# Optimization experiments

Measured on AMD Instinct MI355X. Metric: run time of the kernel, lower is better.

Reference implementation:

```python
import jax, jax.numpy as jnp
import numpy as np

# ParamsJR('JR') defaults, all variances 0 -> fixed constants; w_bb and lm are the fit params.
DT = 1e-4                      # step_size
VMAX, V0, R = 5.0, 6.0, 0.56   # sigmoid params
U_UB = 500.0                   # u_2ndsys_ub
G_EFF = 0.01 + 1000.0          # lb + relu(g)
C1_EFF, C2_EFF = 0.01 + 135.0, 0.01 + 135.0 * 0.8
C3_EFF, C4_EFF = 0.01 + 135.0 * 0.25, 0.01 + 135.0 * 0.25
STD_EFF = 150.0 + 100.0        # noise_std_lb + relu(std_in)
K_EFF = 0.5 + 5.0              # k_lb + relu(k)
A_EFF, a_EFF = 3.25, 1.0 + 100.0   # 0+relu(A), 1+relu(a)
B_EFF, b_EFF = 22.0, 1.0 + 50.0    # 0+relu(B), 1+relu(b)
CY0, Y0, MU = 5.0, 2.0, 0.5
CONDUCT_LB = 1.5


def _sig(x):
    return VMAX / (1.0 + jnp.exp(R * (V0 - x)))


def _sys2nd(A, a, u, x, v):
    return A * a * u - 2.0 * a * v - a * a * x


def _sat(x):  # state saturation 1000*tanh(x/1000)
    return 1000.0 * jnp.tanh(x / 1000.0)


def setup_inputs() -> dict:
    N, H, B, OUT, BUF = 200, 20, 400, 64, 500
    key = jax.random.key(0)
    ks = jax.random.split(key, 7)
    return {
        "input": jax.random.normal(ks[0], (N, H, B), jnp.float32),
        "noise_in": jax.random.normal(ks[1], (N, H, B, 3), jnp.float32),
        "noise_out": jax.random.normal(ks[2], (N, B), jnp.float32),
        "hx": jax.random.uniform(ks[3], (N, 6), jnp.float32),
        "hE": jnp.zeros((N, BUF), jnp.float32),
        "w_bb": jnp.full((N, N), 0.05, jnp.float32),  # zeros + 0.05 init
        "lm": jax.random.normal(ks[4], (OUT, N), jnp.float32),
        "sc": jax.random.uniform(ks[5], (N, N), jnp.float32),
        "dist": jax.random.randint(ks[6], (N, N), 0, 100, dtype=jnp.int32),
    }


def _forward(input, noise_in, noise_out, hx, hE, w_bb, lm, sc, delays):
    OUT = lm.shape[0]
    # connectivity normalization (done once, outside the time loop, as in torch)
    w = jnp.exp(w_bb) * sc
    wl = jnp.log1p(0.5 * (w + w.T))
    w_n = wl / jnp.linalg.norm(wl)             # (N,N)
    dg = -jnp.diag(jnp.sum(w_n, axis=1))       # (N,N) Laplacian diagonal
    # lead-field normalization: rowwise L1 (torch: sqrt(lm**2).sum(1)), then column mean-center
    lm1 = lm / jnp.abs(lm).sum(axis=1, keepdims=True)
    lm_t = lm1 - lm1.sum(axis=0, keepdims=True) / OUT

    def inner(carry, xs):
        M, E, I, Mv, Ev, Iv, hEb = carry
        u, nE = xs                                              # (N,1) each
        Ed = jnp.take_along_axis(hEb, delays, axis=1)           # delayed M buffer
        LEd = jnp.sum(w_n * Ed.T, axis=1, keepdims=True)        # (N,1)
        rM = _sig(E - I)
        rE = STD_EFF * nE + G_EFF * (LEd + dg @ E) + C2_EFF * _sig(C1_EFF * M)
        rI = C4_EFF * _sig(C3_EFF * M)
        ddM = M + DT * Mv
        ddE = E + DT * Ev
        ddI = I + DT * Iv
        ddMv = Mv + DT * _sys2nd(A_EFF, a_EFF, U_UB * jnp.tanh(rM / U_UB), M, Mv)
        ddEv = Ev + DT * _sys2nd(A_EFF, a_EFF, K_EFF * u + U_UB * jnp.tanh(rE / U_UB), E, Ev)
        ddIv = Iv + DT * _sys2nd(B_EFF, b_EFF, U_UB * jnp.tanh(rI / U_UB), I, Iv)
        M, E, I = _sat(ddM), _sat(ddE), _sat(ddI)
        Mv, Ev, Iv = _sat(ddMv), _sat(ddEv), _sat(ddIv)
        hEb = hEb.at[:, 0].set(M[:, 0])
        return (M, E, I, Mv, Ev, Iv, hEb), None

    def outer(carry, xs):
        u_tr, n_tr = xs                                         # (H,N,1) each
        carry, _ = jax.lax.scan(inner, carry, (u_tr, n_tr))
        M, E, I, Mv, Ev, Iv, hEb = carry
        hEb = jnp.concatenate([M, hEb[:, :-1]], axis=1)         # shift delay buffer per TR
        eeg = CY0 * (lm_t @ (E - I)) - Y0                       # (OUT,1)
        return (M, E, I, Mv, Ev, Iv, hEb), eeg[:, 0]

    M, E, I = hx[:, 0:1], hx[:, 1:2], hx[:, 2:3]
    Mv, Ev, Iv = hx[:, 3:4], hx[:, 4:5], hx[:, 5:6]
    u_all = jnp.transpose(input, (2, 1, 0))[..., None]          # (B,H,N,1)
    nE_all = jnp.transpose(noise_in[..., 0], (2, 1, 0))[..., None]
    carry, eeg = jax.lax.scan(outer, (M, E, I, Mv, Ev, Iv, hE), (u_all, nE_all))
    M, E, I, Mv, Ev, Iv, _ = carry
    current_state = jnp.concatenate([M, E, I, Mv, Ev, Iv], axis=1)  # (N,6)
    return eeg.T, current_state                                 # eeg_batch (OUT,B)


def reference(input, noise_in, noise_out, hx, hE, w_bb, lm, sc, dist):
    delays = (dist.astype(jnp.float32) / (CONDUCT_LB + MU)).astype(jnp.int32)
    return _forward(input, noise_in, noise_out, hx, hE, w_bb, lm, sc, delays)
```

## Files before the change

kernel.cpp:

```cpp
#include <hip/hip_runtime.h>
#include <math.h>

namespace {

constexpr int N_   = 200;
constexpr int H_   = 20;
constexpr int B_   = 400;
constexpr int OUT_ = 64;
constexpr int BUF_ = 500;
constexpr int NT_  = 1024;
constexpr int HD_  = 50;
constexpr int HS_  = 51;
constexpr int GT0  = 224;
constexpr int NG_  = 800;
constexpr int EPT  = 50;
constexpr int CAP  = 16;
constexpr int UNR  = 12;

constexpr float L2E = 1.4426950408889634f;
constexpr float LN2 = 0.6931471805599453f;

constexpr float DT_  = 0.0001f;
constexpr float G_   = 1000.01f;
constexpr float C1_  = 135.01f;
constexpr float C2_  = 108.01f;
constexpr float C3_  = 33.76f;
constexpr float C4_  = 33.76f;
constexpr float STD_ = 250.0f;
constexpr float K_   = 5.5f;
constexpr float CY0_ = 5.0f;
constexpr float Y0_  = 2.0f;

constexpr float RL2E = 0.56f * L2E;
constexpr float V0R  = 6.0f * RL2E;
constexpr float TU_  = 2.0f * L2E / 500.0f;
constexpr float TS_  = 2.0f * L2E / 1000.0f;

constexpr float KMv = 0.9798f, KMu = 0.0328250f, KMx = 1.0201f;
constexpr float KEv = 0.9798f, KEu = 0.0328250f, KEx = 1.0201f;
constexpr float KIv = 0.9898f, KIu = 0.1122000f, KIx = 0.2601f;

__device__ __forceinline__ float fexp2(float x){ return __builtin_amdgcn_exp2f(x); }
__device__ __forceinline__ float flog2(float x){ return __builtin_amdgcn_logf(x); }
__device__ __forceinline__ float frcp (float x){ return __builtin_amdgcn_rcpf(x); }

__device__ __forceinline__ float sigf(float x){
    return 5.0f * frcp(1.0f + fexp2(fmaf(-RL2E, x, V0R)));
}
__device__ __forceinline__ float tanh500(float x){
    return 500.0f - 1000.0f * frcp(1.0f + fexp2(x * TU_));
}
__device__ __forceinline__ float satf(float x){
    return 1000.0f - 2000.0f * frcp(1.0f + fexp2(x * TS_));
}
__device__ __forceinline__ float wl_f(const float* __restrict__ wbb,
                                      const float* __restrict__ sc,
                                      int i, int j){
    float w0 = fexp2(wbb[i*N_+j]*L2E) * sc[i*N_+j];
    float w1 = fexp2(wbb[j*N_+i]*L2E) * sc[j*N_+i];
    return flog2(1.0f + 0.5f*(w0+w1)) * LN2;
}

__global__ void __launch_bounds__(NT_)
jansen_kernel(
    const float* __restrict__ input,
    const float* __restrict__ noise_in,
    const float* __restrict__ hx,
    const float* __restrict__ hEin,
    const float* __restrict__ wbb,
    const float* __restrict__ lm,
    const float* __restrict__ sc,
    const int*   __restrict__ dist,
    float* __restrict__ out,
    float2* __restrict__ tab)
{
    __shared__ float histT[N_*HS_];
    __shared__ float uslab[H_*N_];
    __shared__ float neslab[H_*N_];
    __shared__ float d0w_l[CAP*N_];
    __shared__ unsigned char d0j_l[CAP*N_];
    __shared__ float d1w_l[CAP*N_];
    __shared__ unsigned char d1j_l[CAP*N_];
    __shared__ float led_part[4*N_];
    __shared__ float mcol[2*N_];
    __shared__ float emi[N_];
    __shared__ float colmean[N_];
    __shared__ float lmrs[OUT_];
    __shared__ float red_s[NT_/64];
    __shared__ float norm_s;

    const int t = threadIdx.x;
    const bool isr = (t < N_);
    const bool isg = (t >= GT0);
    const int  gt  = t - GT0;
    const int  grow  = gt >> 2;
    const int  gslot = gt & 3;
    const int  jbase = gslot * EPT;
    const int  tb    = gt * EPT;

    int sidx[5];
    int goff[5];

    if (t < OUT_){
        float s2 = 0.f;
        for (int j=0;j<N_;++j) s2 += fabsf(lm[t*N_+j]);
        lmrs[t] = s2;
    }
    float M=0,E=0,I=0,Mv=0,Ev=0,Iv=0, rowsum=0, ledst=0;
    int cnt0=0, cnt1=0;
    #pragma unroll
    for (int r=0;r<5;++r){ sidx[r]=0; goff[r]=0; }
    if (isg){
        #pragma unroll
        for (int r=0;r<5;++r){
            int p = r*NG_ + gt;
            int hh = p / N_, ii = p - hh*N_;
            sidx[r] = hh*N_ + ii;
            goff[r] = ii*(H_*B_) + hh*B_;
            uslab[sidx[r]]  = input[goff[r]];
            neslab[sidx[r]] = noise_in[goff[r]*3];
        }
    }
    if (isr){
        for (int k=1;k<HD_;++k) histT[t*HS_ + (HD_-k)] = hEin[t*BUF_+k];
        mcol[t] = hEin[t*BUF_];
        M=hx[t*6+0]; E=hx[t*6+1]; I=hx[t*6+2];
        Mv=hx[t*6+3]; Ev=hx[t*6+4]; Iv=hx[t*6+5];
    }
    __syncthreads();

    float ss = 0.f, rs = 0.f;
    for (int m=0;m<EPT;++m){
        float w = 0.f; int d = 2;
        int j = jbase + m;
        if (isg){
            d = dist[j*N_+grow] >> 1;
            w = wl_f(wbb, sc, grow, j);
        }
        ss = fmaf(w,w,ss); rs += w;
        if (isg){
            int dm = (d<2) ? 2 : d;
            float ws = (d>=2) ? w : 0.f;
            tab[tb+m] = make_float2(ws, __uint_as_float((unsigned)j | ((unsigned)dm<<16)));
        }
    }
    if (isr){
        float cm=0.f;
        for (int o=0;o<OUT_;++o) cm += lm[o*N_+t] * frcp(lmrs[o]);
        colmean[t] = cm * (1.0f/(float)OUT_);
    }
    #pragma unroll
    for (int o=32;o>0;o>>=1) ss += __shfl_down(ss,o,64);
    if ((t&63)==0) red_s[t>>6] = ss;
    __syncthreads();
    if (t==0){ float tot=0.f; for (int w=0;w<NT_/64;++w) tot+=red_s[w]; norm_s = sqrtf(tot); }
    __syncthreads();
    const float inv = 1.0f / norm_s;
    if (isg){
        float* tf = (float*)tab;
        for (int m=0;m<EPT;++m) tf[2*(tb+m)] *= inv;
    }
    if (isg) led_part[gslot*N_+grow] = rs;

    float dw[UNR]; unsigned jpk[3];
    #pragma unroll
    for (int k=0;k<UNR;++k) dw[k] = 0.f;
    jpk[0]=jpk[1]=jpk[2]=0u;
    if (isr){
        #pragma unroll
        for (int k=0;k<UNR;++k){ d0w_l[k*N_+t]=0.f; d0j_l[k*N_+t]=0;
                                 d1w_l[k*N_+t]=0.f; d1j_l[k*N_+t]=0; }
        for (int j=0;j<N_;++j){
            int dd = dist[j*N_+t] >> 1;
            if (dd < 2){
                float w = wl_f(wbb, sc, t, j) * inv;
                if (dd==0){ if (cnt0<CAP){ d0w_l[cnt0*N_+t]=w; d0j_l[cnt0*N_+t]=(unsigned char)j; ++cnt0; } }
                else      { if (cnt1<CAP){ d1w_l[cnt1*N_+t]=w; d1j_l[cnt1*N_+t]=(unsigned char)j; ++cnt1; } }
            }
        }
        #pragma unroll
        for (int k=0;k<UNR;++k){
            dw[k] = d0w_l[k*N_+t];
            unsigned jv = d0j_l[k*N_+t];
            jpk[k>>2] |= jv << ((k&3)*8);
        }
    }
    __syncthreads();

    if (isr){
        rowsum = (led_part[t]+led_part[N_+t]+led_part[2*N_+t]+led_part[3*N_+t]) * inv;
    }
    __syncthreads();

    if (isg){
        float a0 = 0.f;
        for (int m=0;m<EPT;++m){
            float2 e = tab[tb+m];
            unsigned um = __float_as_uint(e.y);
            int c = HD_ - (int)(um>>16);
            a0 = fmaf(e.x, histT[(um&0xFFFFu)*HS_ + c], a0);
        }
        led_part[gslot*N_+grow] = a0;
    }
    __syncthreads();

    if (isr){
        float v = led_part[t]+led_part[N_+t]+led_part[2*N_+t]+led_part[3*N_+t];
        #pragma unroll
        for (int k=0;k<UNR;++k)
            v = fmaf(d1w_l[k*N_+t], histT[(int)d1j_l[k*N_+t]*HS_ + 49], v);
        for (int k=UNR;k<cnt1;++k)
            v = fmaf(d1w_l[k*N_+t], histT[(int)d1j_l[k*N_+t]*HS_ + 49], v);
        ledst = v;
    }
    __syncthreads();

#define ROW_BODY(MCR, MCW, HH)                                               \
    do {                                                                     \
        float rM  = sigf(E - I);                                             \
        float uM  = tanh500(rM);                                             \
        float Mn  = satf(fmaf(DT_, Mv, M));                                  \
        float Mvn = satf(fmaf(KMv, Mv, fmaf(KMu, uM, -KMx*M)));              \
        (MCW)[t] = Mn;                                                       \
        float rI  = C4_*sigf(C3_*M);                                         \
        float uI  = tanh500(rI);                                             \
        float In  = satf(fmaf(DT_, Iv, I));                                  \
        float Ivn = satf(fmaf(KIv, Iv, fmaf(KIu, uI, -KIx*I)));              \
        float u  = uslab[(HH)*N_+t];                                         \
        float ne = neslab[(HH)*N_+t];                                        \
        float l0 = ledst, l1 = 0.f, l2 = 0.f, l3 = 0.f;                      \
        _Pragma("unroll")                                                    \
        for (int k=0;k<UNR;++k){                                             \
            int j = (jpk[k>>2] >> ((k&3)*8)) & 255;                          \
            float v = (MCR)[j];                                              \
            if      ((k&3)==0) l0 = fmaf(dw[k], v, l0);                      \
            else if ((k&3)==1) l1 = fmaf(dw[k], v, l1);                      \
            else if ((k&3)==2) l2 = fmaf(dw[k], v, l2);                      \
            else               l3 = fmaf(dw[k], v, l3);                      \
        }                                                                    \
        for (int k=UNR;k<cnt0;++k)                                           \
            l0 = fmaf(d0w_l[k*N_+t], (MCR)[d0j_l[k*N_+t]], l0);              \
        float LEd = (l0+l1)+(l2+l3);                                         \
        float rE  = fmaf(STD_, ne, G_*(LEd - rowsum*E)) + C2_*sigf(C1_*M);   \
        float uE  = fmaf(K_, u, tanh500(rE));                                \
        float En  = satf(fmaf(DT_, Ev, E));                                  \
        float Evn = satf(fmaf(KEv, Ev, fmaf(KEu, uE, -KEx*E)));              \
        M=Mn; Mv=Mvn; I=In; Iv=Ivn; E=En; Ev=Evn;                            \
    } while(0)

#define GUSE(W, Mt)                                                         \
    do {                                                                     \
        unsigned um = __float_as_uint(Mt);                                   \
        int c = ts - (int)(um>>16); if (c<0) c += HD_;                       \
        acc = fmaf((W), histT[(um&0xFFFFu)*HS_ + c], acc);                   \
    } while(0)

    float pw0=0,pm0=0,pw1=0,pm1=0;
    float tw0=0,tm0=0,tw1=0,tm1=0,tw2=0,tm2=0;
    if (isg){
        float2 e0 = tab[tb+0]; pw0=e0.x; pm0=e0.y;
        float2 e1 = tab[tb+1]; pw1=e1.x; pm1=e1.y;
    }

    int smod = 0;
    for (int s=0; s<B_; ++s){
        int ts = smod+1; if (ts==HD_) ts = 0;
        float acc = 0.f;
        for (int q=0; q<10; ++q){
            if (isg){
                GUSE(pw0, pm0);
                GUSE(pw1, pm1);
                float2 e;
                e = tab[tb + 5*q + 2]; tw0=e.x; tm0=e.y;
                e = tab[tb + 5*q + 3]; tw1=e.x; tm1=e.y;
                e = tab[tb + 5*q + 4]; tw2=e.x; tm2=e.y;
            }
            if (isr) ROW_BODY(mcol, mcol+N_, 2*q);
            __syncthreads();
            if (isg){
                GUSE(tw0, tm0);
                GUSE(tw1, tm1);
                GUSE(tw2, tm2);
                int nb = (q==9) ? 0 : 5*(q+1);
                float2 e;
                e = tab[tb + nb];     pw0=e.x; pm0=e.y;
                e = tab[tb + nb + 1]; pw1=e.x; pm1=e.y;
            }
            if (isr) ROW_BODY(mcol+N_, mcol, 2*q+1);
            __syncthreads();
        }
        if (isr){ histT[t*HS_ + smod] = M; emi[t] = E - I; }
        if (isg){
            led_part[gslot*N_+grow] = acc;
            int sn = s+1; if (sn >= B_) sn = B_-1;
            #pragma unroll
            for (int r=0;r<5;++r){
                uslab[sidx[r]]  = input[goff[r] + sn];
                neslab[sidx[r]] = noise_in[(goff[r] + sn)*3];
            }
        }
        __syncthreads();
        if (isr){
            float v = led_part[t]+led_part[N_+t]+led_part[2*N_+t]+led_part[3*N_+t];
            #pragma unroll
            for (int k=0;k<UNR;++k)
                v = fmaf(d1w_l[k*N_+t], mcol[d1j_l[k*N_+t]], v);
            for (int k=UNR;k<cnt1;++k)
                v = fmaf(d1w_l[k*N_+t], mcol[d1j_l[k*N_+t]], v);
            ledst = v;
        }
        {
            int o = t>>4, l = t&15;
            float il = frcp(lmrs[o]);
            float a2 = 0.f;
            for (int j=l;j<N_;j+=16)
                a2 = fmaf(fmaf(lm[o*N_+j], il, -colmean[j]), emi[j], a2);
            a2 += __shfl_down(a2,8,16); a2 += __shfl_down(a2,4,16);
            a2 += __shfl_down(a2,2,16); a2 += __shfl_down(a2,1,16);
            if (l==0) out[o*B_+s] = fmaf(CY0_, a2, -Y0_);
        }
        smod = ts;
        __syncthreads();
    }

#undef ROW_BODY
#undef GUSE

    if (isr){
        float* cs = out + OUT_*B_ + t*6;
        cs[0]=M; cs[1]=E; cs[2]=I; cs[3]=Mv; cs[4]=Ev; cs[5]=Iv;
    }
}

}

extern "C" void kernel_launch(void* const* d_in, const int* in_sizes, int n_in,
                              void* d_out, int out_size, void* d_ws, size_t ws_size,
                              hipStream_t stream)
{
    const float* input    = (const float*)d_in[0];
    const float* noise_in = (const float*)d_in[1];
    const float* hx   = (const float*)d_in[3];
    const float* hEin = (const float*)d_in[4];
    const float* wbb  = (const float*)d_in[5];
    const float* lm   = (const float*)d_in[6];
    const float* sc   = (const float*)d_in[7];
    const int*   dist = (const int*)d_in[8];
    float* out = (float*)d_out;
    float2* tab = (float2*)((char*)d_ws + 1024);

    hipLaunchKernelGGL(jansen_kernel, dim3(1), dim3(NT_), 0, stream,
                       input, noise_in, hx, hEin, wbb, lm, sc, dist, out, tab);
}
```

Before: 6.519 ms.

## Advance three inner steps per barrier by recomputing neighbour M trajectories locally

Each row thread now advances three inner time steps per block barrier instead of one. It reads a float4 snapshot of each delay-0 neighbour's state (M, Mv, E-I) and recomputes that neighbour's next two M values itself, so the barrier count per outer step drops from 20 to 7. The neighbour's recomputed M depends only on its own M, Mv and E-I, so the result matches the one-step-per-barrier order. Input and noise slabs are packed into a float2 array, and the gather side processes 8 table entries per phase instead of 5. The cost is redundant per-neighbour sigmoid, tanh and saturation work on the serial row-thread path, plus larger shared-memory reads.

```diff
diff --git a/kernel.cpp b/kernel.cpp
--- a/kernel.cpp
+++ b/kernel.cpp
@@ -74,20 +74,19 @@
     float* __restrict__ out,
     float2* __restrict__ tab)
 {
-    __shared__ float histT[N_*HS_];
-    __shared__ float uslab[H_*N_];
-    __shared__ float neslab[H_*N_];
-    __shared__ float d0w_l[CAP*N_];
+    __shared__ float  histT[N_*HS_];
+    __shared__ float2 une[H_*N_];
+    __shared__ float4 snap2[2*N_];
+    __shared__ float  d0w_l[CAP*N_];
     __shared__ unsigned char d0j_l[CAP*N_];
-    __shared__ float d1w_l[CAP*N_];
+    __shared__ float  d1w_l[CAP*N_];
     __shared__ unsigned char d1j_l[CAP*N_];
-    __shared__ float led_part[4*N_];
-    __shared__ float mcol[2*N_];
-    __shared__ float emi[N_];
-    __shared__ float colmean[N_];
-    __shared__ float lmrs[OUT_];
-    __shared__ float red_s[NT_/64];
-    __shared__ float norm_s;
+    __shared__ float  led_part[4*N_];
+    __shared__ float  emi[N_];
+    __shared__ float  colmean[N_];
+    __shared__ float  lmrs[OUT_];
+    __shared__ float  red_s[NT_/64];
+    __shared__ float  norm_s;
 
     const int t = threadIdx.x;
     const bool isr = (t < N_);
@@ -117,15 +116,14 @@
             int hh = p / N_, ii = p - hh*N_;
             sidx[r] = hh*N_ + ii;
             goff[r] = ii*(H_*B_) + hh*B_;
-            uslab[sidx[r]]  = input[goff[r]];
-            neslab[sidx[r]] = noise_in[goff[r]*3];
+            une[sidx[r]] = make_float2(input[goff[r]], noise_in[goff[r]*3]);
         }
     }
     if (isr){
         for (int k=1;k<HD_;++k) histT[t*HS_ + (HD_-k)] = hEin[t*BUF_+k];
-        mcol[t] = hEin[t*BUF_];
         M=hx[t*6+0]; E=hx[t*6+1]; I=hx[t*6+2];
         Mv=hx[t*6+3]; Ev=hx[t*6+4]; Iv=hx[t*6+5];
+        snap2[t] = make_float4(hEin[t*BUF_], Mv, E - I, M);
     }
     __syncthreads();
 
@@ -215,79 +213,82 @@
     }
     __syncthreads();
 
-#define ROW_BODY(MCR, MCW, HH)                                               \
-    do {                                                                     \
-        float rM  = sigf(E - I);                                             \
-        float uM  = tanh500(rM);                                             \
-        float Mn  = satf(fmaf(DT_, Mv, M));                                  \
-        float Mvn = satf(fmaf(KMv, Mv, fmaf(KMu, uM, -KMx*M)));              \
-        (MCW)[t] = Mn;                                                       \
-        float rI  = C4_*sigf(C3_*M);                                         \
-        float uI  = tanh500(rI);                                             \
-        float In  = satf(fmaf(DT_, Iv, I));                                  \
-        float Ivn = satf(fmaf(KIv, Iv, fmaf(KIu, uI, -KIx*I)));              \
-        float u  = uslab[(HH)*N_+t];                                         \
-        float ne = neslab[(HH)*N_+t];                                        \
-        float l0 = ledst, l1 = 0.f, l2 = 0.f, l3 = 0.f;                      \
-        _Pragma("unroll")                                                    \
-        for (int k=0;k<UNR;++k){                                             \
-            int j = (jpk[k>>2] >> ((k&3)*8)) & 255;                          \
-            float v = (MCR)[j];                                              \
-            if      ((k&3)==0) l0 = fmaf(dw[k], v, l0);                      \
-            else if ((k&3)==1) l1 = fmaf(dw[k], v, l1);                      \
-            else if ((k&3)==2) l2 = fmaf(dw[k], v, l2);                      \
-            else               l3 = fmaf(dw[k], v, l3);                      \
-        }                                                                    \
-        for (int k=UNR;k<cnt0;++k)                                           \
-            l0 = fmaf(d0w_l[k*N_+t], (MCR)[d0j_l[k*N_+t]], l0);              \
-        float LEd = (l0+l1)+(l2+l3);                                         \
-        float rE  = fmaf(STD_, ne, G_*(LEd - rowsum*E)) + C2_*sigf(C1_*M);   \
-        float uE  = fmaf(K_, u, tanh500(rE));                                \
-        float En  = satf(fmaf(DT_, Ev, E));                                  \
-        float Evn = satf(fmaf(KEv, Ev, fmaf(KEu, uE, -KEx*E)));              \
-        M=Mn; Mv=Mvn; I=In; Iv=Ivn; E=En; Ev=Evn;                            \
-    } while(0)
-
-#define GUSE(W, Mt)                                                         \
-    do {                                                                     \
-        unsigned um = __float_as_uint(Mt);                                   \
-        int c = ts - (int)(um>>16); if (c<0) c += HD_;                       \
-        acc = fmaf((W), histT[(um&0xFFFFu)*HS_ + c], acc);                   \
-    } while(0)
-
-    float pw0=0,pm0=0,pw1=0,pm1=0;
-    float tw0=0,tm0=0,tw1=0,tm1=0,tw2=0,tm2=0;
-    if (isg){
-        float2 e0 = tab[tb+0]; pw0=e0.x; pm0=e0.y;
-        float2 e1 = tab[tb+1]; pw1=e1.x; pm1=e1.y;
-    }
+#define STEP(LEDV, UN) do{                                                   \
+    float rM  = sigf(E - I);                                                 \
+    float uM  = tanh500(rM);                                                 \
+    float Mn  = satf(fmaf(DT_, Mv, M));                                      \
+    float Mvn = satf(fmaf(KMv, Mv, fmaf(KMu, uM, -KMx*M)));                  \
+    float rI  = C4_*sigf(C3_*M);                                             \
+    float uI  = tanh500(rI);                                                 \
+    float In  = satf(fmaf(DT_, Iv, I));                                      \
+    float Ivn = satf(fmaf(KIv, Iv, fmaf(KIu, uI, -KIx*I)));                  \
+    float rE  = fmaf(STD_, (UN).y, G_*((LEDV) - rowsum*E)) + C2_*sigf(C1_*M);\
+    float uE  = fmaf(K_, (UN).x, tanh500(rE));                               \
+    float En  = satf(fmaf(DT_, Ev, E));                                      \
+    float Evn = satf(fmaf(KEv, Ev, fmaf(KEu, uE, -KEx*E)));                  \
+    M=Mn; Mv=Mvn; I=In; Iv=Ivn; E=En; Ev=Evn;                                \
+}while(0)
+
+#define REP(W, SJ, LA, LB, LC) do{                                           \
+    float Mj1  = satf(fmaf(DT_, (SJ).y, (SJ).w));                            \
+    float uMj  = tanh500(sigf((SJ).z));                                      \
+    float Mvj1 = satf(fmaf(KMv, (SJ).y, fmaf(KMu, uMj, -KMx*(SJ).w)));       \
+    float Mj2  = satf(fmaf(DT_, Mvj1, Mj1));                                 \
+    LA = fmaf((W), (SJ).x, LA);                                              \
+    LB = fmaf((W), Mj1,    LB);                                              \
+    LC = fmaf((W), Mj2,    LC);                                              \
+}while(0)
 
     int smod = 0;
+    int pp = 0;
     for (int s=0; s<B_; ++s){
         int ts = smod+1; if (ts==HD_) ts = 0;
         float acc = 0.f;
-        for (int q=0; q<10; ++q){
+        for (int q=0; q<7; ++q){
+            const int h0  = 3*q;
+            const bool full = (q < 6);
             if (isg){
-                GUSE(pw0, pm0);
-                GUSE(pw1, pm1);
-                float2 e;
-                e = tab[tb + 5*q + 2]; tw0=e.x; tm0=e.y;
-                e = tab[tb + 5*q + 3]; tw1=e.x; tm1=e.y;
-                e = tab[tb + 5*q + 4]; tw2=e.x; tm2=e.y;
+                const int mb = q*8;
+                #pragma unroll
+                for (int k=0;k<8;++k){
+                    if (full || k<2){
+                        float2 e = tab[tb+mb+k];
+                        unsigned um = __float_as_uint(e.y);
+                        int c = ts - (int)(um>>16); if (c<0) c += HD_;
+                        acc = fmaf(e.x, histT[(um&0xFFFFu)*HS_ + c], acc);
+                    }
+                }
             }
-            if (isr) ROW_BODY(mcol, mcol+N_, 2*q);
+            if (isr){
+                const float4* sr = &snap2[pp*N_];
+                float4*       sw = &snap2[(pp^1)*N_];
+                float2 un0 = une[(h0+0)*N_+t];
+                float2 un1 = une[(h0+1)*N_+t];
+                float2 un2 = full ? une[(h0+2)*N_+t] : make_float2(0.f,0.f);
+                float lA0=0,lA1=0,lB0=0,lB1=0,lC0=0,lC1=0;
+                #pragma unroll
+                for (int k=0;k<UNR;++k){
+                    int j = (jpk[k>>2] >> ((k&3)*8)) & 255;
+                    float w = dw[k];
+                    float4 sj = sr[j];
+                    if (k&1) REP(w, sj, lA1, lB1, lC1);
+                    else     REP(w, sj, lA0, lB0, lC0);
+                }
+                for (int k=UNR;k<cnt0;++k){
+                    float w = d0w_l[k*N_+t];
+                    float4 sj = sr[d0j_l[k*N_+t]];
+                    REP(w, sj, lA0, lB0, lC0);
+                }
+                float LA = ledst + (lA0+lA1);
+                float LB = ledst + (lB0+lB1);
+                float LC = ledst + (lC0+lC1);
+                STEP(LA, un0);
+                STEP(LB, un1);
+                if (full) STEP(LC, un2);
+                sw[t] = make_float4(M, Mv, E - I, M);
+            }
             __syncthreads();
-            if (isg){
-                GUSE(tw0, tm0);
-                GUSE(tw1, tm1);
-                GUSE(tw2, tm2);
-                int nb = (q==9) ? 0 : 5*(q+1);
-                float2 e;
-                e = tab[tb + nb];     pw0=e.x; pm0=e.y;
-                e = tab[tb + nb + 1]; pw1=e.x; pm1=e.y;
-            }
-            if (isr) ROW_BODY(mcol+N_, mcol, 2*q+1);
-            __syncthreads();
+            pp ^= 1;
         }
         if (isr){ histT[t*HS_ + smod] = M; emi[t] = E - I; }
         if (isg){
@@ -295,18 +296,19 @@
             int sn = s+1; if (sn >= B_) sn = B_-1;
             #pragma unroll
             for (int r=0;r<5;++r){
-                uslab[sidx[r]]  = input[goff[r] + sn];
-                neslab[sidx[r]] = noise_in[(goff[r] + sn)*3];
+                une[sidx[r]] = make_float2(input[goff[r] + sn],
+                                           noise_in[(goff[r] + sn)*3]);
             }
         }
         __syncthreads();
         if (isr){
             float v = led_part[t]+led_part[N_+t]+led_part[2*N_+t]+led_part[3*N_+t];
+            const float4* sp = &snap2[pp*N_];
             #pragma unroll
             for (int k=0;k<UNR;++k)
-                v = fmaf(d1w_l[k*N_+t], mcol[d1j_l[k*N_+t]], v);
+                v = fmaf(d1w_l[k*N_+t], sp[d1j_l[k*N_+t]].w, v);
             for (int k=UNR;k<cnt1;++k)
-                v = fmaf(d1w_l[k*N_+t], mcol[d1j_l[k*N_+t]], v);
+                v = fmaf(d1w_l[k*N_+t], sp[d1j_l[k*N_+t]].w, v);
             ledst = v;
         }
         {
@@ -323,8 +325,8 @@
         __syncthreads();
     }
 
-#undef ROW_BODY
-#undef GUSE
+#undef STEP
+#undef REP
 
     if (isr){
         float* cs = out + OUT_*B_ + t*6;
```

Measured after the change: 11.52 ms. +76.8%, slower.
